# Kernel tuning notes

Hardware: AMD Instinct MI355X
Metric: run time of the kernel (lower is better)

The kernel has to match this reference:

```python
import jax, jax.numpy as jnp
import numpy as np

B, S, N_NODES, D_IN = 8, 24, 400, 3
D_MODEL = 32
G1_HEADS, G1_DIM = 4, 16
G2_HEADS, G2_DIM = 1, 32
T_KEY = 32


def _ln(x, g, b, eps=1e-6):
    m = jnp.mean(x, -1, keepdims=True)
    v = jnp.var(x, -1, keepdims=True)
    return g * (x - m) / jnp.sqrt(v + eps) + b


def _gat(x, adj, wq, bq, wk, bk, wv, bv, heads, dim):
    # x: [B*, N, F]; adjacency-masked multi-head attention (GraphAttention)
    Bx, N, _ = x.shape
    q = (x @ wq + bq).reshape(Bx, N, heads, dim)
    k = (x @ wk + bk).reshape(Bx, N, heads, dim)
    v = (x @ wv + bv).reshape(Bx, N, heads, dim)
    s = jnp.einsum('bihd,bjhd->bhij', q, k) / jnp.sqrt(jnp.float32(dim))
    s = jnp.where((adj == 0)[None, None], jnp.float32(-1e9), s)
    w = jax.nn.softmax(s, axis=-1)
    o = jnp.einsum('bhij,bjhd->bihd', w, v)
    return o.reshape(Bx, N, heads * dim)


def _mha(x, wq, bq, wk, bk, wv, bv, wo, bo):
    # keras MultiHeadAttention(num_heads=2, key_dim=32), self-attention, output dim = 32
    q = jnp.einsum('bsd,dhk->bshk', x, wq) + bq
    k = jnp.einsum('bsd,dhk->bshk', x, wk) + bk
    v = jnp.einsum('bsd,dhk->bshk', x, wv) + bv
    a = jax.nn.softmax(jnp.einsum('bqhk,bshk->bhqs', q, k) / jnp.sqrt(jnp.float32(T_KEY)), axis=-1)
    o = jnp.einsum('bhqs,bshk->bqhk', a, v)
    return jnp.einsum('bqhk,hko->bqo', o, wo) + bo


def setup_inputs() -> dict:
    ks = jax.random.split(jax.random.key(0), 20)

    def w(k, shape, scale=0.05):
        return (jax.random.normal(k, shape) * scale).astype(jnp.float32)

    z = lambda *s: jnp.zeros(s, jnp.float32)
    one = lambda *s: jnp.ones(s, jnp.float32)

    d = {}
    d['inputs'] = jax.random.normal(ks[0], (B, S, N_NODES, D_IN), dtype=jnp.float32)
    adj = (jax.random.uniform(ks[1], (N_NODES, N_NODES)) < 0.05).astype(jnp.float32)
    adj = jnp.minimum(adj + jnp.eye(N_NODES, dtype=jnp.float32), 1.0)
    d['adj'] = adj / (jnp.sum(adj, axis=1, keepdims=True) + 1e-6)  # row-normalized

    d['g1_wq'] = w(ks[2], (D_IN, G1_HEADS * G1_DIM)); d['g1_bq'] = z(G1_HEADS * G1_DIM)
    d['g1_wk'] = w(ks[3], (D_IN, G1_HEADS * G1_DIM)); d['g1_bk'] = z(G1_HEADS * G1_DIM)
    d['g1_wv'] = w(ks[4], (D_IN, G1_HEADS * G1_DIM)); d['g1_bv'] = z(G1_HEADS * G1_DIM)
    d['g2_wq'] = w(ks[5], (G1_HEADS * G1_DIM, G2_DIM)); d['g2_bq'] = z(G2_DIM)
    d['g2_wk'] = w(ks[6], (G1_HEADS * G1_DIM, G2_DIM)); d['g2_bk'] = z(G2_DIM)
    d['g2_wv'] = w(ks[7], (G1_HEADS * G1_DIM, G2_DIM)); d['g2_bv'] = z(G2_DIM)
    d['sp_g'] = one(D_MODEL); d['sp_b'] = z(D_MODEL)
    d['t_wq'] = w(ks[8], (D_MODEL, 2, T_KEY)); d['t_bq'] = z(2, T_KEY)
    d['t_wk'] = w(ks[9], (D_MODEL, 2, T_KEY)); d['t_bk'] = z(2, T_KEY)
    d['t_wv'] = w(ks[10], (D_MODEL, 2, T_KEY)); d['t_bv'] = z(2, T_KEY)
    d['t_wo'] = w(ks[11], (2, T_KEY, D_MODEL)); d['t_bo'] = z(D_MODEL)
    d['ff_w1'] = w(ks[12], (D_MODEL, 64)); d['ff_b1'] = z(64)
    d['ff_w2'] = w(ks[13], (64, D_MODEL)); d['ff_b2'] = z(D_MODEL)
    d['ln1_g'] = one(D_MODEL); d['ln1_b'] = z(D_MODEL)
    d['ln2_g'] = one(D_MODEL); d['ln2_b'] = z(D_MODEL)
    d['fin_g'] = one(D_MODEL); d['fin_b'] = z(D_MODEL)
    d['fd_w'] = w(ks[14], (D_MODEL, 1), scale=0.01); d['fd_b'] = z(1)
    return d


def reference(inputs, adj, g1_wq, g1_bq, g1_wk, g1_bk, g1_wv, g1_bv,
              g2_wq, g2_bq, g2_wk, g2_bk, g2_wv, g2_bv, sp_g, sp_b,
              t_wq, t_bq, t_wk, t_bk, t_wv, t_bv, t_wo, t_bo,
              ff_w1, ff_b1, ff_w2, ff_b2, ln1_g, ln1_b, ln2_g, ln2_b,
              fin_g, fin_b, fd_w, fd_b):
    Bx, Sx, N, _ = inputs.shape
    x = inputs.reshape(Bx * Sx, N, D_IN)

    # SpatialProcessor: GAT1 -> relu -> GAT2 -> residual layernorm
    h = jax.nn.relu(_gat(x, adj, g1_wq, g1_bq, g1_wk, g1_bk, g1_wv, g1_bv, G1_HEADS, G1_DIM))
    h = _gat(h, adj, g2_wq, g2_bq, g2_wk, g2_bk, g2_wv, g2_bv, G2_HEADS, G2_DIM)
    res = jnp.pad(x, ((0, 0), (0, 0), (0, D_MODEL - D_IN)))  # zero-pad 3 -> 32 for residual
    sp = _ln(h + res, sp_g, sp_b)
    sp4 = sp.reshape(Bx, Sx, N, D_MODEL)  # [B, S, N, 32]

    # TemporalTransformer over sequence per node
    t_in = jnp.transpose(sp4, (0, 2, 1, 3)).reshape(Bx * N, Sx, D_MODEL)
    a = _mha(t_in, t_wq, t_bq, t_wk, t_bk, t_wv, t_bv, t_wo, t_bo)
    x1 = _ln(t_in + a, ln1_g, ln1_b)
    f = jax.nn.gelu(x1 @ ff_w1 + ff_b1, approximate=False) @ ff_w2 + ff_b2
    t_out = _ln(x1 + f, ln2_g, ln2_b).reshape(Bx, N, Sx, D_MODEL)

    # fuse: mean over seq (spatial) + mean over seq (temporal), layernorm, final dense
    fused = _ln(jnp.mean(sp4, axis=1) + jnp.mean(t_out, axis=2), fin_g, fin_b)
    return (fused @ fd_w + fd_b)[..., 0]  # [B, N]
```

## Files before the change

kernel.cpp:

```cpp
#include <hip/hip_runtime.h>
#include <hip/hip_bf16.h>

#define NN 400
#define KMAX 64

struct WTab {
  const void* p[34];
  int off[35];
};

__device__ __forceinline__ float bflo(unsigned u) {
  union { unsigned i; float f; } x; x.i = u << 16; return x.f;
}
__device__ __forceinline__ float bfhi(unsigned u) {
  union { unsigned i; float f; } x; x.i = u & 0xffff0000u; return x.f;
}
__device__ __forceinline__ unsigned short f2bf(float f) {
  __hip_bfloat16 b = __float2bfloat16(f);
  return *reinterpret_cast<unsigned short*>(&b);
}
__device__ __forceinline__ unsigned packbf(float a, float b) {
  return (unsigned)f2bf(a) | ((unsigned)f2bf(b) << 16);
}
__device__ __forceinline__ bool detect_bf16(const unsigned short* probe) {
  int lane = threadIdx.x & 63;
  unsigned short u = probe[lane * 2];
  int e = (u >> 7) & 0xFF;
  bool plaus = (u == 0) || (e >= 112 && e <= 132);
  return __popcll(__ballot(plaus)) >= 48;
}
__device__ __forceinline__ float rsum32(float v) {
  v += __shfl_xor(v, 1); v += __shfl_xor(v, 2); v += __shfl_xor(v, 4);
  v += __shfl_xor(v, 8); v += __shfl_xor(v, 16); return v;
}

__global__ __launch_bounds__(256) void prep_k(
    WTab wt, const void* __restrict__ adj,
    const unsigned short* __restrict__ probe, float* __restrict__ dst,
    int* __restrict__ colp, int* __restrict__ degp) {
  bool isbf = detect_bf16(probe);
  const int tid = threadIdx.x;
  if (blockIdx.x < 40) {
    int total = wt.off[34];
    for (int i = blockIdx.x * 256 + tid; i < total; i += 40 * 256) {
      int lo = 0, hi = 33;
      while (lo < hi) {
        int mid = (lo + hi + 1) >> 1;
        if (i >= wt.off[mid]) lo = mid; else hi = mid - 1;
      }
      int rel = i - wt.off[lo];
      float v;
      if (isbf) v = __bfloat162float(((const __hip_bfloat16*)wt.p[lo])[rel]);
      else      v = ((const float*)wt.p[lo])[rel];
      dst[i] = v;
    }
  } else {
    int row = (blockIdx.x - 40) * 4 + (tid >> 6);
    int lane = tid & 63;
    int base = 0;
    for (int j0 = 0; j0 < NN; j0 += 64) {
      int j = j0 + lane;
      bool nz;
      if (isbf) nz = (j < NN) && ((const unsigned short*)adj)[row * NN + j] != 0;
      else      nz = (j < NN) && ((const float*)adj)[row * NN + j] != 0.0f;
      unsigned long long m = __ballot(nz);
      int offl = __popcll(m & ((1ull << lane) - 1ull));
      if (nz) {
        int pidx = base + offl;
        if (pidx < KMAX) colp[row * KMAX + pidx] = j;
      }
      base += __popcll(m);
    }
    if (lane == 0) degp[row] = base < KMAX ? base : KMAX;
  }
}

__global__ __launch_bounds__(256) void gat1proj_k(
    const void* __restrict__ xraw, const unsigned short* __restrict__ probe,
    const float* __restrict__ g1, const float* __restrict__ g2,
    const int* __restrict__ colp, const int* __restrict__ degp,
    unsigned short* __restrict__ q2b, unsigned short* __restrict__ k2g,
    unsigned short* __restrict__ v2g) {
  __shared__ __align__(16) float smf[8832];
  float* xsf = smf;
  float* yhf = smf + 1600;
  float* w1s = smf + 8000;
  float* cf  = smf + 8768;
  unsigned short* ht = (unsigned short*)smf;
  const int tid = threadIdx.x;
  const int g = blockIdx.x;
  const int i0 = blockIdx.y * 200;
  bool isbf = detect_bf16(probe);

  for (int e = tid; e < 768; e += 256) w1s[e] = g1[e];
  for (int e = tid; e < NN; e += 256) xsf[e * 4 + 3] = 0.f;
  for (int e = tid; e < NN * 3; e += 256) {
    int j = e / 3, a = e - j * 3;
    float v;
    if (isbf) v = __bfloat162float(((const __hip_bfloat16*)xraw)[g * NN * 3 + e]);
    else      v = ((const float*)xraw)[g * NN * 3 + e];
    xsf[j * 4 + a] = v;
  }
  __syncthreads();

  if (tid < 64) {
    int h = tid >> 4, t = tid & 15, co = h * 16;
    float acc = 0.f;
    if (t < 9) {
      int a = t / 3, b = t - (t / 3) * 3;
      for (int c = 0; c < 16; ++c) acc += w1s[a * 64 + co + c] * w1s[256 + b * 64 + co + c];
    } else if (t < 12) {
      int a = t - 9;
      for (int c = 0; c < 16; ++c) acc += w1s[a * 64 + co + c] * w1s[448 + co + c];
    } else if (t < 15) {
      int b = t - 12;
      for (int c = 0; c < 16; ++c) acc += w1s[256 + b * 64 + co + c] * w1s[192 + co + c];
    } else {
      for (int c = 0; c < 16; ++c) acc += w1s[192 + co + c] * w1s[448 + co + c];
    }
    cf[h * 16 + t] = acc;
  }
  __syncthreads();

  for (int e = tid; e < NN * 4; e += 256) {
    int j = e >> 2, h = e & 3;
    const float* bse = cf + h * 16;
    float x0 = xsf[j * 4], x1 = xsf[j * 4 + 1], x2 = xsf[j * 4 + 2];
    float* y = yhf + (h * NN + j) * 4;
    y[0] = bse[0] * x0 + bse[1] * x1 + bse[2] * x2;
    y[1] = bse[3] * x0 + bse[4] * x1 + bse[5] * x2;
    y[2] = bse[6] * x0 + bse[7] * x1 + bse[8] * x2;
    y[3] = bse[12] * x0 + bse[13] * x1 + bse[14] * x2 + bse[15];
  }
  __syncthreads();

  const float4* xs4 = (const float4*)xsf;
  const float4* yh4 = (const float4*)yhf;
  float bx[4], by[4], bz[4];
  const bool act = tid < 200;
  const int i = i0 + tid;
  if (act) {
    float4 xi = xs4[i];
    float ch[4];
    #pragma unroll
    for (int h = 0; h < 4; ++h)
      ch[h] = cf[h * 16 + 9] * xi.x + cf[h * 16 + 10] * xi.y + cf[h * 16 + 11] * xi.z;
    float l[4] = {0.f, 0.f, 0.f, 0.f};
    #pragma unroll
    for (int h = 0; h < 4; ++h) { bx[h] = 0.f; by[h] = 0.f; bz[h] = 0.f; }
    int dg = degp[i];
    const int* cols = colp + i * KMAX;
    for (int e = 0; e < dg; ++e) {
      int j = cols[e];
      float4 xj = xs4[j];
      #pragma unroll
      for (int h = 0; h < 4; ++h) {
        float4 y = yh4[h * NN + j];
        float s = (xi.x * y.x + xi.y * y.y + xi.z * y.z + y.w + ch[h]) * 0.25f;
        float p = __expf(s);
        l[h] += p;
        bx[h] += p * xj.x; by[h] += p * xj.y; bz[h] += p * xj.z;
      }
    }
    #pragma unroll
    for (int h = 0; h < 4; ++h) {
      float inv = 1.f / l[h];
      bx[h] *= inv; by[h] *= inv; bz[h] *= inv;
    }
  }
  __syncthreads();

  if (act) {
    #pragma unroll
    for (int h = 0; h < 4; ++h) {
      int co = h * 16;
      #pragma unroll
      for (int c = 0; c < 16; ++c) {
        int d = co + c;
        float hd = fmaxf(bx[h] * w1s[512 + d] + by[h] * w1s[576 + d] +
                         bz[h] * w1s[640 + d] + w1s[704 + d], 0.f);
        ht[d * 208 + tid] = f2bf(hd);
      }
    }
  }
  __syncthreads();

  {
    const int c = tid & 31, ng = tid >> 5;
    const float* wq = g2;
    const float* wk = g2 + 2080;
    const float* wv = g2 + 4160;
    const float bq = g2[2048 + c], bk = g2[4128 + c], bv = g2[6208 + c];
    for (int base = 0; base < 200; base += 64) {
      const int nb = base + ng * 8;
      if (nb < 200) {
        float qa[8], ka[8], va[8];
        #pragma unroll
        for (int k = 0; k < 8; ++k) { qa[k] = bq; ka[k] = bk; va[k] = bv; }
        for (int d = 0; d < 64; ++d) {
          float wqv = wq[d * 32 + c], wkv = wk[d * 32 + c], wvv = wv[d * 32 + c];
          uint4 hv4 = *(const uint4*)(ht + d * 208 + nb);
          unsigned uu[4] = {hv4.x, hv4.y, hv4.z, hv4.w};
          #pragma unroll
          for (int m = 0; m < 4; ++m) {
            float h0 = bflo(uu[m]), h1v = bfhi(uu[m]);
            qa[2*m] += h0 * wqv;   qa[2*m+1] += h1v * wqv;
            ka[2*m] += h0 * wkv;   ka[2*m+1] += h1v * wkv;
            va[2*m] += h0 * wvv;   va[2*m+1] += h1v * wvv;
          }
        }
        #pragma unroll
        for (int k = 0; k < 8; ++k) {
          size_t gn = (size_t)g * NN + i0 + nb + k;
          q2b[gn * 32 + c] = f2bf(qa[k]);
          k2g[gn * 32 + c] = f2bf(ka[k]);
          v2g[gn * 32 + c] = f2bf(va[k]);
        }
      }
    }
  }
}

__global__ __launch_bounds__(256) void gat2_attn_k(
    const void* __restrict__ xraw, const unsigned short* __restrict__ probe,
    const unsigned short* __restrict__ q2b, const unsigned short* __restrict__ k2g,
    const unsigned short* __restrict__ v2g, const float* __restrict__ spw,
    const int* __restrict__ colp, const int* __restrict__ degp,
    float* __restrict__ spo) {
  __shared__ unsigned short k2s[NN * 40];
  __shared__ unsigned short v2s[NN * 40];
  __shared__ float gw[64];
  const int tid = threadIdx.x;
  const int g = blockIdx.x;
  bool isbf = detect_bf16(probe);
  if (tid < 64) gw[tid] = spw[tid];
  for (int e = tid; e < 3200; e += 256) {
    uint2 uk = ((const uint2*)k2g)[g * 3200 + e];
    uint2 uv = ((const uint2*)v2g)[g * 3200 + e];
    int n = e >> 3, c = (e & 7) * 2;
    *(uint2*)((unsigned*)k2s + n * 20 + c) = uk;
    *(uint2*)((unsigned*)v2s + n * 20 + c) = uv;
  }
  __syncthreads();
  const int b = g / 24, st = g % 24;
  const int i0 = blockIdx.y * 200;
  for (int i = i0 + tid; i < i0 + 200; i += 256) {
    const uint4* qp = (const uint4*)(q2b + ((size_t)g * NN + i) * 32);
    uint4 qw[4] = {qp[0], qp[1], qp[2], qp[3]};
    float q[32], o[32];
    #pragma unroll
    for (int t = 0; t < 4; ++t) {
      unsigned uu[4] = {qw[t].x, qw[t].y, qw[t].z, qw[t].w};
      #pragma unroll
      for (int m = 0; m < 4; ++m) {
        q[t * 8 + 2 * m] = bflo(uu[m]); q[t * 8 + 2 * m + 1] = bfhi(uu[m]);
      }
    }
    #pragma unroll
    for (int c = 0; c < 32; ++c) o[c] = 0.f;
    int dg = degp[i];
    const int* cols = colp + i * KMAX;
    float l = 0.f;
    for (int e = 0; e < dg; ++e) {
      int j = cols[e];
      const uint4* kr = (const uint4*)(k2s + j * 40);
      const uint4* vr = (const uint4*)(v2s + j * 40);
      float s = 0.f;
      #pragma unroll
      for (int t = 0; t < 4; ++t) {
        uint4 kk = kr[t];
        unsigned uu[4] = {kk.x, kk.y, kk.z, kk.w};
        #pragma unroll
        for (int m = 0; m < 4; ++m)
          s += q[t * 8 + 2 * m] * bflo(uu[m]) + q[t * 8 + 2 * m + 1] * bfhi(uu[m]);
      }
      float p = __expf(s * 0.17677669529663688f);
      l += p;
      #pragma unroll
      for (int t = 0; t < 4; ++t) {
        uint4 vv = vr[t];
        unsigned uu[4] = {vv.x, vv.y, vv.z, vv.w};
        #pragma unroll
        for (int m = 0; m < 4; ++m) {
          o[t * 8 + 2 * m]     += p * bflo(uu[m]);
          o[t * 8 + 2 * m + 1] += p * bfhi(uu[m]);
        }
      }
    }
    float inv = 1.f / l;
    float xr[3];
    #pragma unroll
    for (int a = 0; a < 3; ++a) {
      if (isbf) xr[a] = __bfloat162float(((const __hip_bfloat16*)xraw)[((size_t)g * NN + i) * 3 + a]);
      else      xr[a] = ((const float*)xraw)[((size_t)g * NN + i) * 3 + a];
    }
    float row[32];
    #pragma unroll
    for (int c = 0; c < 32; ++c) row[c] = o[c] * inv;
    row[0] += xr[0]; row[1] += xr[1]; row[2] += xr[2];
    float mean = 0.f;
    #pragma unroll
    for (int c = 0; c < 32; ++c) mean += row[c];
    mean *= (1.f / 32.f);
    float var = 0.f;
    #pragma unroll
    for (int c = 0; c < 32; ++c) { float dd = row[c] - mean; var += dd * dd; }
    var *= (1.f / 32.f);
    float rinv = 1.f / sqrtf(var + 1e-6f);
    float4* so4 = (float4*)(spo + (((size_t)b * NN + i) * 24 + st) * 32);
    #pragma unroll
    for (int k = 0; k < 8; ++k) {
      float4 v;
      v.x = gw[4 * k]     * (row[4 * k]     - mean) * rinv + gw[32 + 4 * k];
      v.y = gw[4 * k + 1] * (row[4 * k + 1] - mean) * rinv + gw[33 + 4 * k];
      v.z = gw[4 * k + 2] * (row[4 * k + 2] - mean) * rinv + gw[34 + 4 * k];
      v.w = gw[4 * k + 3] * (row[4 * k + 3] - mean) * rinv + gw[35 + 4 * k];
      so4[k] = v;
    }
  }
}

__global__ __launch_bounds__(192) void temporal_k(
    const float* __restrict__ sp, const float* __restrict__ tw,
    const unsigned short* __restrict__ probe, void* __restrict__ outp) {
  __shared__ float sm[6648];
  float* t_s = sm;
  float* q_s = sm + 768;
  float* k_s = sm + 2328;
  float* v_s = sm + 3888;
  float* aw  = sm + 5448;
  float* x1s = sm + 5448;
  float* att = q_s;
  float* f1s = k_s;
  float* tos = v_s;
  const int tid = threadIdx.x;
  bool isbf = detect_bf16(probe);

  const float* twq = tw;            const float* tbq = tw + 2048;
  const float* twk = tw + 2112;     const float* tbk = tw + 4160;
  const float* twv = tw + 4224;     const float* tbv = tw + 6272;
  const float* two = tw + 6336;     const float* tbo = tw + 8384;
  const float* fw1 = tw + 8416;     const float* fb1 = tw + 10464;
  const float* fw2 = tw + 10528;    const float* fb2 = tw + 12576;
  const float* l1g = tw + 12608;    const float* l1b = tw + 12640;
  const float* l2g = tw + 12672;    const float* l2b = tw + 12704;
  const float* fng = tw + 12736;    const float* fnb = tw + 12768;
  const float* fdw = tw + 12800;    const float* fdb = tw + 12832;

  const float4* base4 = (const float4*)(sp + (size_t)blockIdx.x * 768);
  for (int e = tid; e < 192; e += 192) ((float4*)t_s)[e] = base4[e];
  __syncthreads();

  {
    const int hk = tid & 63, a = tid >> 6;
    const float* W  = (a == 0) ? twq : (a == 1) ? twk : twv;
    const float* Bb = (a == 0) ? tbq : (a == 1) ? tbk : tbv;
    float* dst      = (a == 0) ? q_s : (a == 1) ? k_s : v_s;
    float w[32];
    #pragma unroll
    for (int c = 0; c < 32; ++c) w[c] = W[c * 64 + hk];
    float bias = Bb[hk];
    for (int s = 0; s < 24; ++s) {
      float acc = bias;
      const float* tr = t_s + s * 32;
      #pragma unroll
      for (int c = 0; c < 32; ++c) acc += tr[c] * w[c];
      dst[s * 65 + hk] = acc;
    }
  }
  __syncthreads();

  if (tid < 96) {
    const int h = tid / 48, rem = tid % 48, qs = rem >> 1, half = rem & 1;
    const float* qr = q_s + qs * 65 + h * 32;
    float sc[12], l = 0.f;
    #pragma unroll
    for (int k = 0; k < 12; ++k) {
      const float* kr = k_s + (half * 12 + k) * 65 + h * 32;
      float s = 0.f;
      #pragma unroll
      for (int d = 0; d < 32; ++d) s += qr[d] * kr[d];
      sc[k] = __expf(s * 0.17677669529663688f);
      l += sc[k];
    }
    l += __shfl_xor(l, 1);
    float inv = 1.f / l;
    float* ar = aw + (h * 24 + qs) * 25 + half * 12;
    #pragma unroll
    for (int k = 0; k < 12; ++k) ar[k] = sc[k] * inv;
  }
  __syncthreads();

  for (int e = tid; e < 1536; e += 192) {
    int qs = e >> 6, hk = e & 63, h = hk >> 5;
    const float* ar = aw + (h * 24 + qs) * 25;
    float a = 0.f;
    #pragma unroll
    for (int ss = 0; ss < 24; ++ss) a += ar[ss] * v_s[ss * 65 + hk];
    att[qs * 65 + hk] = a;
  }
  __syncthreads();

  for (int e = tid; e < 768; e += 192) {
    int s = e >> 5, c = e & 31;
    const float* ar = att + s * 65;
    float a = tbo[c];
    #pragma unroll 8
    for (int hk = 0; hk < 64; ++hk) a += ar[hk] * two[hk * 32 + c];
    x1s[s * 33 + c] = t_s[e] + a;
  }
  __syncthreads();
  if (tid < 24) {
    float* r = x1s + tid * 33;
    float mean = 0.f;
    for (int c = 0; c < 32; ++c) mean += r[c];
    mean *= (1.f / 32.f);
    float var = 0.f;
    for (int c = 0; c < 32; ++c) { float d = r[c] - mean; var += d * d; }
    var *= (1.f / 32.f);
    float ri = 1.f / sqrtf(var + 1e-6f);
    for (int c = 0; c < 32; ++c) r[c] = l1g[c] * (r[c] - mean) * ri + l1b[c];
  }
  __syncthreads();

  {
    const int j = tid & 63, sh = tid >> 6;
    float w[32];
    #pragma unroll
    for (int c = 0; c < 32; ++c) w[c] = fw1[c * 64 + j];
    float bias = fb1[j];
    for (int s = sh * 8; s < sh * 8 + 8; ++s) {
      float acc = bias;
      const float* xr = x1s + s * 33;
      #pragma unroll
      for (int c = 0; c < 32; ++c) acc += xr[c] * w[c];
      f1s[s * 64 + j] = 0.5f * acc * (1.f + erff(acc * 0.70710678118654752f));
    }
  }
  __syncthreads();

  for (int e = tid; e < 768; e += 192) {
    int s = e >> 5, c = e & 31;
    const float* fr = f1s + s * 64;
    float a = fb2[c];
    #pragma unroll 8
    for (int j = 0; j < 64; ++j) a += fr[j] * fw2[j * 32 + c];
    tos[s * 33 + c] = x1s[s * 33 + c] + a;
  }
  __syncthreads();
  if (tid < 24) {
    float* r = tos + tid * 33;
    float mean = 0.f;
    for (int c = 0; c < 32; ++c) mean += r[c];
    mean *= (1.f / 32.f);
    float var = 0.f;
    for (int c = 0; c < 32; ++c) { float d = r[c] - mean; var += d * d; }
    var *= (1.f / 32.f);
    float ri = 1.f / sqrtf(var + 1e-6f);
    for (int c = 0; c < 32; ++c) r[c] = l2g[c] * (r[c] - mean) * ri + l2b[c];
  }
  __syncthreads();

  if (tid < 32) {
    const int c = tid;
    float ms = 0.f, mt = 0.f;
    #pragma unroll
    for (int s = 0; s < 24; ++s) { ms += t_s[s * 32 + c]; mt += tos[s * 33 + c]; }
    float red = (ms + mt) * (1.f / 24.f);
    float mean = rsum32(red) * (1.f / 32.f);
    float dv = red - mean;
    float var = rsum32(dv * dv) * (1.f / 32.f);
    float ri = 1.f / sqrtf(var + 1e-6f);
    float y = (fng[c] * dv * ri + fnb[c]) * fdw[c];
    float tot = rsum32(y);
    if (c == 0) {
      float acc = tot + fdb[0];
      if (isbf) ((__hip_bfloat16*)outp)[blockIdx.x] = __float2bfloat16(acc);
      else      ((float*)outp)[blockIdx.x] = acc;
    }
  }
}

extern "C" void kernel_launch(void* const* d_in, const int* in_sizes, int n_in,
                              void* d_out, int out_size, void* d_ws, size_t ws_size,
                              hipStream_t stream) {
  static const int wsizes[34] = {
      192, 64, 192, 64, 192, 64,
      2048, 32, 2048, 32, 2048, 32,
      32, 32,
      2048, 64, 2048, 64, 2048, 64, 2048, 32,
      2048, 64, 2048, 32,
      32, 32, 32, 32, 32, 32,
      32, 1};
  WTab wt;
  int off = 0;
  for (int i = 0; i < 34; ++i) { wt.p[i] = d_in[i + 2]; wt.off[i] = off; off += wsizes[i]; }
  wt.off[34] = off;

  char* ws = (char*)d_ws;
  float* convw = (float*)ws;
  int*   colp  = (int*)(ws + 81920);
  int*   degp  = (int*)(ws + 184320);
  unsigned short* q2b = (unsigned short*)(ws + 196608);
  unsigned short* k2g = (unsigned short*)(ws + 5242880);
  unsigned short* v2g = (unsigned short*)(ws + 10289152);
  float*          spo = (float*)(ws + 15335424);

  const float* g1  = convw;
  const float* g2  = convw + 768;
  const float* spw = convw + 7008;
  const float* twp = convw + 7072;
  const unsigned short* probe = (const unsigned short*)d_in[0];

  hipLaunchKernelGGL(prep_k, dim3(140), dim3(256), 0, stream, wt, d_in[1], probe,
                     convw, colp, degp);
  hipLaunchKernelGGL(gat1proj_k, dim3(192, 2), dim3(256), 0, stream, d_in[0],
                     probe, g1, g2, (const int*)colp, (const int*)degp,
                     q2b, k2g, v2g);
  hipLaunchKernelGGL(gat2_attn_k, dim3(192, 2), dim3(256), 0, stream, d_in[0],
                     probe, (const unsigned short*)q2b, (const unsigned short*)k2g,
                     (const unsigned short*)v2g, spw, (const int*)colp,
                     (const int*)degp, spo);
  hipLaunchKernelGGL(temporal_k, dim3(3200), dim3(192), 0, stream,
                     (const float*)spo, twp, probe, d_out);
}
```

Before: 290.1 us.

## Fuse GAT2 attention and spatial layernorm into temporal kernel per node

Removes the separate GAT2 attention kernel and computes each node's GAT2 output for all 24 timesteps inside the temporal kernel, with one lane per channel and warp-shuffle reductions for scores and layernorm. This drops the fp32 round trip of the spatial output through global memory and one kernel launch. In exchange, K and V rows are gathered straight from global memory rather than staged in shared memory, and each edge's dot product now needs a 32-lane shuffle reduction, which raises gather traffic and latency.

```diff
diff --git a/kernel.cpp b/kernel.cpp
--- a/kernel.cpp
+++ b/kernel.cpp
@@ -15,12 +15,12 @@
 __device__ __forceinline__ float bfhi(unsigned u) {
   union { unsigned i; float f; } x; x.i = u & 0xffff0000u; return x.f;
 }
+__device__ __forceinline__ float bfu16(unsigned short u) {
+  union { unsigned i; float f; } x; x.i = ((unsigned)u) << 16; return x.f;
+}
 __device__ __forceinline__ unsigned short f2bf(float f) {
   __hip_bfloat16 b = __float2bfloat16(f);
   return *reinterpret_cast<unsigned short*>(&b);
-}
-__device__ __forceinline__ unsigned packbf(float a, float b) {
-  return (unsigned)f2bf(a) | ((unsigned)f2bf(b) << 16);
 }
 __device__ __forceinline__ bool detect_bf16(const unsigned short* probe) {
   int lane = threadIdx.x & 63;
@@ -221,108 +221,12 @@
   }
 }
 
-__global__ __launch_bounds__(256) void gat2_attn_k(
+__global__ __launch_bounds__(192) void temporal_k(
     const void* __restrict__ xraw, const unsigned short* __restrict__ probe,
     const unsigned short* __restrict__ q2b, const unsigned short* __restrict__ k2g,
     const unsigned short* __restrict__ v2g, const float* __restrict__ spw,
     const int* __restrict__ colp, const int* __restrict__ degp,
-    float* __restrict__ spo) {
-  __shared__ unsigned short k2s[NN * 40];
-  __shared__ unsigned short v2s[NN * 40];
-  __shared__ float gw[64];
-  const int tid = threadIdx.x;
-  const int g = blockIdx.x;
-  bool isbf = detect_bf16(probe);
-  if (tid < 64) gw[tid] = spw[tid];
-  for (int e = tid; e < 3200; e += 256) {
-    uint2 uk = ((const uint2*)k2g)[g * 3200 + e];
-    uint2 uv = ((const uint2*)v2g)[g * 3200 + e];
-    int n = e >> 3, c = (e & 7) * 2;
-    *(uint2*)((unsigned*)k2s + n * 20 + c) = uk;
-    *(uint2*)((unsigned*)v2s + n * 20 + c) = uv;
-  }
-  __syncthreads();
-  const int b = g / 24, st = g % 24;
-  const int i0 = blockIdx.y * 200;
-  for (int i = i0 + tid; i < i0 + 200; i += 256) {
-    const uint4* qp = (const uint4*)(q2b + ((size_t)g * NN + i) * 32);
-    uint4 qw[4] = {qp[0], qp[1], qp[2], qp[3]};
-    float q[32], o[32];
-    #pragma unroll
-    for (int t = 0; t < 4; ++t) {
-      unsigned uu[4] = {qw[t].x, qw[t].y, qw[t].z, qw[t].w};
-      #pragma unroll
-      for (int m = 0; m < 4; ++m) {
-        q[t * 8 + 2 * m] = bflo(uu[m]); q[t * 8 + 2 * m + 1] = bfhi(uu[m]);
-      }
-    }
-    #pragma unroll
-    for (int c = 0; c < 32; ++c) o[c] = 0.f;
-    int dg = degp[i];
-    const int* cols = colp + i * KMAX;
-    float l = 0.f;
-    for (int e = 0; e < dg; ++e) {
-      int j = cols[e];
-      const uint4* kr = (const uint4*)(k2s + j * 40);
-      const uint4* vr = (const uint4*)(v2s + j * 40);
-      float s = 0.f;
-      #pragma unroll
-      for (int t = 0; t < 4; ++t) {
-        uint4 kk = kr[t];
-        unsigned uu[4] = {kk.x, kk.y, kk.z, kk.w};
-        #pragma unroll
-        for (int m = 0; m < 4; ++m)
-          s += q[t * 8 + 2 * m] * bflo(uu[m]) + q[t * 8 + 2 * m + 1] * bfhi(uu[m]);
-      }
-      float p = __expf(s * 0.17677669529663688f);
-      l += p;
-      #pragma unroll
-      for (int t = 0; t < 4; ++t) {
-        uint4 vv = vr[t];
-        unsigned uu[4] = {vv.x, vv.y, vv.z, vv.w};
-        #pragma unroll
-        for (int m = 0; m < 4; ++m) {
-          o[t * 8 + 2 * m]     += p * bflo(uu[m]);
-          o[t * 8 + 2 * m + 1] += p * bfhi(uu[m]);
-        }
-      }
-    }
-    float inv = 1.f / l;
-    float xr[3];
-    #pragma unroll
-    for (int a = 0; a < 3; ++a) {
-      if (isbf) xr[a] = __bfloat162float(((const __hip_bfloat16*)xraw)[((size_t)g * NN + i) * 3 + a]);
-      else      xr[a] = ((const float*)xraw)[((size_t)g * NN + i) * 3 + a];
-    }
-    float row[32];
-    #pragma unroll
-    for (int c = 0; c < 32; ++c) row[c] = o[c] * inv;
-    row[0] += xr[0]; row[1] += xr[1]; row[2] += xr[2];
-    float mean = 0.f;
-    #pragma unroll
-    for (int c = 0; c < 32; ++c) mean += row[c];
-    mean *= (1.f / 32.f);
-    float var = 0.f;
-    #pragma unroll
-    for (int c = 0; c < 32; ++c) { float dd = row[c] - mean; var += dd * dd; }
-    var *= (1.f / 32.f);
-    float rinv = 1.f / sqrtf(var + 1e-6f);
-    float4* so4 = (float4*)(spo + (((size_t)b * NN + i) * 24 + st) * 32);
-    #pragma unroll
-    for (int k = 0; k < 8; ++k) {
-      float4 v;
-      v.x = gw[4 * k]     * (row[4 * k]     - mean) * rinv + gw[32 + 4 * k];
-      v.y = gw[4 * k + 1] * (row[4 * k + 1] - mean) * rinv + gw[33 + 4 * k];
-      v.z = gw[4 * k + 2] * (row[4 * k + 2] - mean) * rinv + gw[34 + 4 * k];
-      v.w = gw[4 * k + 3] * (row[4 * k + 3] - mean) * rinv + gw[35 + 4 * k];
-      so4[k] = v;
-    }
-  }
-}
-
-__global__ __launch_bounds__(192) void temporal_k(
-    const float* __restrict__ sp, const float* __restrict__ tw,
-    const unsigned short* __restrict__ probe, void* __restrict__ outp) {
+    const float* __restrict__ tw, void* __restrict__ outp) {
   __shared__ float sm[6648];
   float* t_s = sm;
   float* q_s = sm + 768;
@@ -334,6 +238,7 @@
   float* f1s = k_s;
   float* tos = v_s;
   const int tid = threadIdx.x;
+  const int b = blockIdx.x / NN, n = blockIdx.x % NN;
   bool isbf = detect_bf16(probe);
 
   const float* twq = tw;            const float* tbq = tw + 2048;
@@ -347,8 +252,39 @@
   const float* fng = tw + 12736;    const float* fnb = tw + 12768;
   const float* fdw = tw + 12800;    const float* fdb = tw + 12832;
 
-  const float4* base4 = (const float4*)(sp + (size_t)blockIdx.x * 768);
-  for (int e = tid; e < 192; e += 192) ((float4*)t_s)[e] = base4[e];
+  {
+    const int hw = tid >> 5, c = tid & 31;
+    const int dg = degp[n];
+    const int* cols = colp + n * KMAX;
+    const float g0 = spw[c], b0 = spw[32 + c];
+    #pragma unroll
+    for (int r = 0; r < 4; ++r) {
+      const int s = hw * 4 + r;
+      const size_t gb = (size_t)(b * 24 + s) * NN;
+      float qc = bfu16(q2b[(gb + n) * 32 + c]);
+      float l = 0.f, o = 0.f;
+      for (int e = 0; e < dg; ++e) {
+        int j = cols[e];
+        float kc = bfu16(k2g[(gb + j) * 32 + c]);
+        float sc = rsum32(qc * kc) * 0.17677669529663688f;
+        float p = __expf(sc);
+        l += p;
+        o += p * bfu16(v2g[(gb + j) * 32 + c]);
+      }
+      float row = o / l;
+      if (c < 3) {
+        float xv;
+        if (isbf) xv = __bfloat162float(((const __hip_bfloat16*)xraw)[(gb + n) * 3 + c]);
+        else      xv = ((const float*)xraw)[(gb + n) * 3 + c];
+        row += xv;
+      }
+      float mean = rsum32(row) * (1.f / 32.f);
+      float dv = row - mean;
+      float var = rsum32(dv * dv) * (1.f / 32.f);
+      float ri = 1.f / sqrtf(var + 1e-6f);
+      t_s[s * 32 + c] = g0 * dv * ri + b0;
+    }
+  }
   __syncthreads();
 
   {
@@ -504,7 +440,6 @@
   unsigned short* q2b = (unsigned short*)(ws + 196608);
   unsigned short* k2g = (unsigned short*)(ws + 5242880);
   unsigned short* v2g = (unsigned short*)(ws + 10289152);
-  float*          spo = (float*)(ws + 15335424);
 
   const float* g1  = convw;
   const float* g2  = convw + 768;
@@ -517,10 +452,8 @@
   hipLaunchKernelGGL(gat1proj_k, dim3(192, 2), dim3(256), 0, stream, d_in[0],
                      probe, g1, g2, (const int*)colp, (const int*)degp,
                      q2b, k2g, v2g);
-  hipLaunchKernelGGL(gat2_attn_k, dim3(192, 2), dim3(256), 0, stream, d_in[0],
+  hipLaunchKernelGGL(temporal_k, dim3(3200), dim3(192), 0, stream, d_in[0],
                      probe, (const unsigned short*)q2b, (const unsigned short*)k2g,
                      (const unsigned short*)v2g, spw, (const int*)colp,
-                     (const int*)degp, spo);
-  hipLaunchKernelGGL(temporal_k, dim3(3200), dim3(192), 0, stream,
-                     (const float*)spo, twp, probe, d_out);
-}
+                     (const int*)degp, twp, d_out);
+}
```

Measured after the change: 381.0 us. +31.3%, slower.
